# Kernel tuning notes

Measured on AMD Instinct MI355X. Metric: run time of the kernel, lower is better.

The kernel has to match this reference:

```python
import jax, jax.numpy as jnp
import numpy as np

B, S, D = 2, 2048, 768
H = 12
HD = D // H


def setup_inputs() -> dict:
    key = jax.random.key(0)
    k1, k2, k3 = jax.random.split(key, 3)
    hidden_states = jax.random.normal(k1, (B, S, D), dtype=jnp.float32)
    Wqkv = jax.random.normal(k2, (D, 3 * D), dtype=jnp.float32) * (1.0 / np.sqrt(D))
    bqkv = jnp.zeros((3 * D,), dtype=jnp.float32)
    Wout = jax.random.normal(k3, (D, D), dtype=jnp.float32) * (1.0 / np.sqrt(D))
    bout = jnp.zeros((D,), dtype=jnp.float32)
    return {"hidden_states": hidden_states, "Wqkv": Wqkv, "bqkv": bqkv,
            "Wout": Wout, "bout": bout}


def reference(hidden_states, Wqkv, bqkv, Wout, bout):
    b, s, d = hidden_states.shape
    h, hd = H, HD
    scale = hd ** -0.5
    qkv = hidden_states @ Wqkv + bqkv                      # [b, s, 3d]
    q, k, v = jnp.split(qkv, 3, axis=-1)
    # [b, h, s, hd]
    q = q.reshape(b, s, h, hd).transpose(0, 2, 1, 3)
    k = k.reshape(b, s, h, hd).transpose(0, 2, 1, 3)
    v = v.reshape(b, s, h, hd).transpose(0, 2, 1, 3)
    scores = jnp.einsum('bhqd,bhkd->bhqk', q, k) * scale   # [b, h, s, s]
    causal = jnp.tril(jnp.ones((s, s), dtype=bool))
    scores = jnp.where(causal, scores, -jnp.inf)
    attn = jax.nn.softmax(scores, axis=-1)
    out = jnp.einsum('bhqk,bhkd->bhqd', attn, v)           # [b, h, s, hd]
    out = out.transpose(0, 2, 1, 3).reshape(b, s, d)
    return out @ Wout + bout
```

## Files before the change

kernel.cpp:

```cpp
#include <hip/hip_runtime.h>
#include <hip/hip_bf16.h>

typedef __attribute__((ext_vector_type(8))) short bf16x8;
typedef __attribute__((ext_vector_type(4))) float f32x4;
typedef __attribute__((ext_vector_type(4))) unsigned int u32x4;

#define NB 2
#define NS 2048
#define ND 768
#define NH 12
#define NHD 64
#define N3D 2304
#define NM (NB * NS)

__device__ __forceinline__ unsigned short f2bf(float x) {
    union { float f; unsigned u; } v; v.f = x;
    unsigned r = v.u + 0x7FFFu + ((v.u >> 16) & 1u);
    return (unsigned short)(r >> 16);
}

__device__ __forceinline__ unsigned cvt_pk_bf16(float lo, float hi) {
    unsigned r;
    asm volatile("v_cvt_pk_bf16_f32 %0, %1, %2" : "=v"(r) : "v"(lo), "v"(hi));
    return r;
}

__device__ __forceinline__ void transp_tile(const float* __restrict__ in,
                                            unsigned short* __restrict__ out,
                                            int K, int N, int nt, int kt,
                                            float (*T)[33]) {
    const int n0 = nt * 32, k0 = kt * 32;
    const int r = threadIdx.x >> 3, c4 = (threadIdx.x & 7) * 4;
    float4 v = *reinterpret_cast<const float4*>(&in[(size_t)(k0 + r) * N + n0 + c4]);
    T[r][c4 + 0] = v.x; T[r][c4 + 1] = v.y; T[r][c4 + 2] = v.z; T[r][c4 + 3] = v.w;
    __syncthreads();
    ushort4 o;
    o.x = f2bf(T[c4 + 0][r]); o.y = f2bf(T[c4 + 1][r]);
    o.z = f2bf(T[c4 + 2][r]); o.w = f2bf(T[c4 + 3][r]);
    *reinterpret_cast<ushort4*>(&out[(size_t)(n0 + r) * K + k0 + c4]) = o;
}

__global__ __launch_bounds__(256)
void prep(const float* __restrict__ hs, unsigned short* __restrict__ hsb,
          const float* __restrict__ Wqkv, unsigned short* __restrict__ W1t,
          const float* __restrict__ Wout, unsigned short* __restrict__ W2t) {
    __shared__ float T[32][33];
    const int bid = blockIdx.x;
    if (bid < 3072) {
        const int i = (bid * 256 + threadIdx.x) * 4;
        float4 v = *reinterpret_cast<const float4*>(hs + i);
        ushort4 o;
        o.x = f2bf(v.x); o.y = f2bf(v.y); o.z = f2bf(v.z); o.w = f2bf(v.w);
        *reinterpret_cast<ushort4*>(hsb + i) = o;
    } else if (bid < 3072 + 1728) {
        const int idx = bid - 3072;
        transp_tile(Wqkv, W1t, ND, N3D, idx % 72, idx / 72, T);
    } else {
        const int idx = bid - 4800;
        transp_tile(Wout, W2t, ND, ND, idx % 24, idx / 24, T);
    }
}

__global__ __launch_bounds__(256)
void vtransp(const unsigned short* __restrict__ V, unsigned short* __restrict__ Vt) {
    __shared__ __align__(16) unsigned short T[64][72];
    const int bh = blockIdx.y;
    const int s0 = blockIdx.x * 64;
    const int t = threadIdx.x;
    const unsigned short* src = V + ((size_t)bh * NS + s0) * NHD;
    const int r = t >> 2, cc = (t & 3) * 16;
    *(bf16x8*)&T[r][cc]     = *(const bf16x8*)&src[r * NHD + cc];
    *(bf16x8*)&T[r][cc + 8] = *(const bf16x8*)&src[r * NHD + cc + 8];
    __syncthreads();
    unsigned short* dst = Vt + ((size_t)bh * NHD) * NS + s0;
    const int chunk = t & 7;
#pragma unroll
    for (int h = 0; h < 2; ++h) {
        const int d = (t >> 3) + h * 32;
        bf16x8 v;
#pragma unroll
        for (int e = 0; e < 8; ++e) v[e] = (short)T[chunk * 8 + e][d];
        *(bf16x8*)&dst[(size_t)d * NS + chunk * 8] = v;
    }
}

template<int BM, int BN, int EPI>
__global__ __launch_bounds__(256)
void gemm_k768(const unsigned short* __restrict__ A,
               const unsigned short* __restrict__ Bt,
               const float* __restrict__ bias,
               unsigned short* __restrict__ Qo, unsigned short* __restrict__ Ko,
               unsigned short* __restrict__ Vo, float* __restrict__ Co) {
    __shared__ unsigned short As[BM * 64];
    __shared__ unsigned short Bs[BN * 64];
    const int t = threadIdx.x;
    const int wv = t >> 6, lane = t & 63;
    const int lr = lane & 15, lg = lane >> 4;
    const int wr = wv >> 1, wc = wv & 1;
    const int m0 = blockIdx.y * BM;
    const int n0 = blockIdx.x * BN;
    constexpr int FM = BM / 32;
    constexpr int FN = BN / 32;

    f32x4 acc[FM][FN];
#pragma unroll
    for (int i = 0; i < FM; ++i)
#pragma unroll
        for (int j = 0; j < FN; ++j) acc[i][j] = (f32x4){0.f, 0.f, 0.f, 0.f};

    const int sr = t >> 3;
    const int sb = t & 7;

    for (int ki = 0; ki < ND / 64; ++ki) {
        const int k0 = ki * 64;
        __syncthreads();
#pragma unroll
        for (int jj = 0; jj < BM / 32; ++jj) {
            const int row = jj * 32 + sr;
            __builtin_amdgcn_global_load_lds(
                (const void*)(A + (size_t)(m0 + row) * ND + k0 + ((sb ^ (row & 7)) * 8)),
                (void*)(As + jj * 2048 + wv * 512), 16, 0, 0);
        }
#pragma unroll
        for (int jj = 0; jj < BN / 32; ++jj) {
            const int row = jj * 32 + sr;
            __builtin_amdgcn_global_load_lds(
                (const void*)(Bt + (size_t)(n0 + row) * ND + k0 + ((sb ^ (row & 7)) * 8)),
                (void*)(Bs + jj * 2048 + wv * 512), 16, 0, 0);
        }
        __syncthreads();
#pragma unroll
        for (int kc = 0; kc < 2; ++kc) {
            bf16x8 af[FM], bfr[FN];
#pragma unroll
            for (int mi = 0; mi < FM; ++mi) {
                const int row = wr * (BM / 2) + mi * 16 + lr;
                af[mi] = *(const bf16x8*)&As[row * 64 + (((kc * 4 + lg) ^ (row & 7)) * 8)];
            }
#pragma unroll
            for (int nj = 0; nj < FN; ++nj) {
                const int row = wc * (BN / 2) + nj * 16 + lr;
                bfr[nj] = *(const bf16x8*)&Bs[row * 64 + (((kc * 4 + lg) ^ (row & 7)) * 8)];
            }
#pragma unroll
            for (int mi = 0; mi < FM; ++mi)
#pragma unroll
                for (int nj = 0; nj < FN; ++nj)
                    acc[mi][nj] = __builtin_amdgcn_mfma_f32_16x16x32_bf16(
                        af[mi], bfr[nj], acc[mi][nj], 0, 0, 0);
        }
    }

    if (EPI == 0) {
        const int sec = n0 / ND;
#pragma unroll
        for (int mi = 0; mi < FM; ++mi) {
#pragma unroll
            for (int nj = 0; nj < FN; ++nj) {
                const int n = n0 + wc * (BN / 2) + nj * 16 + lr;
                const int rem = n - sec * ND;
                const int hh = rem >> 6, dd = rem & 63;
                const float b = bias[n];
#pragma unroll
                for (int r = 0; r < 4; ++r) {
                    const int m = m0 + wr * (BM / 2) + mi * 16 + lg * 4 + r;
                    const int bb = m >> 11, ss = m & (NS - 1);
                    const int bhh = bb * NH + hh;
                    const float v = acc[mi][nj][r] + b;
                    if (sec == 0)
                        Qo[((size_t)bhh * NS + ss) * NHD + dd] = f2bf(v * 0.18033688011112042f);
                    else if (sec == 1)
                        Ko[((size_t)bhh * NS + ss) * NHD + dd] = f2bf(v);
                    else
                        Vo[((size_t)bhh * NS + ss) * NHD + dd] = f2bf(v);
                }
            }
        }
    } else {
#pragma unroll
        for (int mi = 0; mi < FM; ++mi)
#pragma unroll
            for (int nj = 0; nj < FN; ++nj) {
                const int n = n0 + wc * (BN / 2) + nj * 16 + lr;
                const float b = bias[n];
#pragma unroll
                for (int r = 0; r < 4; ++r) {
                    const int m = m0 + wr * (BM / 2) + mi * 16 + lg * 4 + r;
                    Co[(size_t)m * ND + n] = acc[mi][nj][r] + b;
                }
            }
    }
}

__global__ __launch_bounds__(256)
void attn_mfma(const unsigned short* __restrict__ Qg,
               const unsigned short* __restrict__ Kg,
               const unsigned short* __restrict__ Vtg,
               unsigned short* __restrict__ AO) {
    __shared__ unsigned short Ks[2][64 * 64];
    __shared__ unsigned short Vs[2][64 * 64];
    const int n = blockIdx.x;
    const int x = n & 7, ii = n >> 3;
    const int bh = ((ii >> 5) << 3) + x;
    const int qt = (31 - (ii & 31) + 11 * (ii >> 5)) & 31;
    const int t = threadIdx.x;
    const int w = t >> 6, lane = t & 63;
    const int lr = lane & 15, lg = lane >> 4;
    const int lgp = lg & 1;
    const int qrow = qt * 64 + w * 16 + lr;
    const size_t bhoff = (size_t)bh * (NS * NHD);

    const unsigned short* Qp = Qg + bhoff + (size_t)qrow * NHD;
    const bf16x8 qB0 = *(const bf16x8*)(Qp + lg * 8);
    const bf16x8 qB1 = *(const bf16x8*)(Qp + 32 + lg * 8);

    float m_run = -1e30f, l_part = 0.f;
    f32x4 of[4];
#pragma unroll
    for (int f = 0; f < 4; ++f) of[f] = (f32x4){0.f, 0.f, 0.f, 0.f};

    const unsigned short* Kb = Kg + bhoff;
    const unsigned short* Vb = Vtg + bhoff;
    const int srow = lane >> 3, sblk = lane & 7;
    const int ntiles = qt + 1;
    const int bswz = ((lg & 1) << 1) | (lg >> 1);

#define STAGE(buf, kv0)                                                           \
    {                                                                             \
        _Pragma("unroll")                                                         \
        for (int h = 0; h < 2; ++h) {                                             \
            const int rr = w * 16 + h * 8 + srow;                                 \
            __builtin_amdgcn_global_load_lds(                                     \
                (const void*)(Kb + (size_t)((kv0) + rr) * NHD + ((sblk ^ (rr & 7)) * 8)),  \
                (void*)(Ks[buf] + (w * 16 + h * 8) * 64), 16, 0, 0);              \
            __builtin_amdgcn_global_load_lds(                                     \
                (const void*)(Vb + (size_t)rr * NS + (kv0) + ((sblk ^ (rr & 7)) * 8)),     \
                (void*)(Vs[buf] + (w * 16 + h * 8) * 64), 16, 0, 0);              \
        }                                                                         \
    }

    STAGE(0, 0);
    for (int kt = 0; kt < ntiles; ++kt) {
        __syncthreads();
        if (kt + 1 < ntiles) STAGE((kt + 1) & 1, (kt + 1) * 64);
        const unsigned short* Kc = Ks[kt & 1];
        const unsigned short* Vc = Vs[kt & 1];
        const int kv0 = kt * 64;

        f32x4 sf[4];
#pragma unroll
        for (int f = 0; f < 4; ++f) sf[f] = (f32x4){0.f, 0.f, 0.f, 0.f};
        __builtin_amdgcn_s_setprio(1);
#pragma unroll
        for (int f = 0; f < 4; ++f) {
            const int krow = f * 16 + lr;
            const bf16x8 a0 = *(const bf16x8*)&Kc[krow * 64 + ((lg ^ (krow & 7)) * 8)];
            const bf16x8 a1 = *(const bf16x8*)&Kc[krow * 64 + (((4 + lg) ^ (krow & 7)) * 8)];
            sf[f] = __builtin_amdgcn_mfma_f32_16x16x32_bf16(a0, qB0, sf[f], 0, 0, 0);
            sf[f] = __builtin_amdgcn_mfma_f32_16x16x32_bf16(a1, qB1, sf[f], 0, 0, 0);
        }
        __builtin_amdgcn_s_setprio(0);

        if (kt == ntiles - 1) {
            const int thr = qrow - kv0;
#pragma unroll
            for (int f = 0; f < 4; ++f)
#pragma unroll
                for (int r = 0; r < 4; ++r)
                    if (f * 16 + lg * 4 + r > thr) sf[f][r] = -1e30f;
        }

        float tm = -1e30f;
#pragma unroll
        for (int f = 0; f < 4; ++f)
            tm = fmaxf(tm, fmaxf(fmaxf(sf[f][0], sf[f][1]), fmaxf(sf[f][2], sf[f][3])));
        tm = fmaxf(tm, __shfl_xor(tm, 16));
        tm = fmaxf(tm, __shfl_xor(tm, 32));
        if (!__all(tm <= m_run)) {
            const float nm = fmaxf(m_run, tm);
            const float corr = exp2f(m_run - nm);
            m_run = nm;
            l_part *= corr;
#pragma unroll
            for (int f = 0; f < 4; ++f)
#pragma unroll
                for (int r = 0; r < 4; ++r) of[f][r] *= corr;
        }
#pragma unroll
        for (int f = 0; f < 4; ++f)
#pragma unroll
            for (int r = 0; r < 4; ++r) {
                sf[f][r] = exp2f(sf[f][r] - m_run);
                l_part += sf[f][r];
            }

        bf16x8 pb[2];
#pragma unroll
        for (int c = 0; c < 2; ++c) {
            const unsigned A0 = cvt_pk_bf16(sf[2 * c][0], sf[2 * c][1]);
            const unsigned A1 = cvt_pk_bf16(sf[2 * c][2], sf[2 * c][3]);
            const unsigned B0 = cvt_pk_bf16(sf[2 * c + 1][0], sf[2 * c + 1][1]);
            const unsigned B1 = cvt_pk_bf16(sf[2 * c + 1][2], sf[2 * c + 1][3]);
            const unsigned s0 = lgp ? A0 : B0;
            const unsigned s1 = lgp ? A1 : B1;
            const unsigned r0 = (unsigned)__shfl_xor((int)s0, 16);
            const unsigned r1 = (unsigned)__shfl_xor((int)s1, 16);
            const unsigned o0 = lgp ? B0 : A0;
            const unsigned o1 = lgp ? B1 : A1;
            u32x4 wvv;
            wvv[0] = lgp ? r0 : o0;
            wvv[1] = lgp ? r1 : o1;
            wvv[2] = lgp ? o0 : r0;
            wvv[3] = lgp ? o1 : r1;
            pb[c] = __builtin_bit_cast(bf16x8, wvv);
        }

        __builtin_amdgcn_s_setprio(1);
#pragma unroll
        for (int fA = 0; fA < 4; ++fA) {
            const int drow = fA * 16 + lr;
#pragma unroll
            for (int c = 0; c < 2; ++c) {
                const int blk = 4 * c + bswz;
                const bf16x8 va = *(const bf16x8*)&Vc[drow * 64 + ((blk ^ (drow & 7)) * 8)];
                of[fA] = __builtin_amdgcn_mfma_f32_16x16x32_bf16(va, pb[c], of[fA], 0, 0, 0);
            }
        }
        __builtin_amdgcn_s_setprio(0);
    }
#undef STAGE

    l_part += __shfl_xor(l_part, 16);
    l_part += __shfl_xor(l_part, 32);
    const float inv = 1.f / l_part;
    const int bb = bh / NH, hh = bh - bb * NH;
    unsigned short* op = AO + ((size_t)(bb * NS + qrow)) * ND + hh * NHD;
#pragma unroll
    for (int fA = 0; fA < 4; ++fA) {
        ushort4 o4;
        o4.x = f2bf(of[fA][0] * inv);
        o4.y = f2bf(of[fA][1] * inv);
        o4.z = f2bf(of[fA][2] * inv);
        o4.w = f2bf(of[fA][3] * inv);
        *reinterpret_cast<ushort4*>(op + fA * 16 + lg * 4) = o4;
    }
}

extern "C" void kernel_launch(void* const* d_in, const int* in_sizes, int n_in,
                              void* d_out, int out_size, void* d_ws, size_t ws_size,
                              hipStream_t stream) {
    const float* hs   = (const float*)d_in[0];
    const float* Wqkv = (const float*)d_in[1];
    const float* bqkv = (const float*)d_in[2];
    const float* Wout = (const float*)d_in[3];
    const float* bout = (const float*)d_in[4];
    float* out = (float*)d_out;

    char* wp = (char*)d_ws;
    unsigned short* hsb = (unsigned short*)wp; wp += (size_t)NM * ND * 2;
    unsigned short* W1t = (unsigned short*)wp; wp += (size_t)N3D * ND * 2;
    unsigned short* W2t = (unsigned short*)wp; wp += (size_t)ND * ND * 2;
    const size_t per = (size_t)NB * NH * NS * NHD;
    unsigned short* Qb  = (unsigned short*)wp; wp += per * 2;
    unsigned short* Kb  = (unsigned short*)wp; wp += per * 2;
    unsigned short* Vtb = (unsigned short*)wp; wp += per * 2;
    unsigned short* AOb = (unsigned short*)wp; wp += per * 2;

    prep<<<3072 + 1728 + 576, 256, 0, stream>>>(hs, hsb, Wqkv, W1t, Wout, W2t);

    gemm_k768<128, 128, 0><<<dim3(N3D / 128, NM / 128), 256, 0, stream>>>(
        hsb, W1t, bqkv, Qb, Kb, AOb, nullptr);

    vtransp<<<dim3(NS / 64, NB * NH), 256, 0, stream>>>(AOb, Vtb);

    attn_mfma<<<dim3(NS / 64 * NB * NH), 256, 0, stream>>>(Qb, Kb, Vtb, AOb);

    gemm_k768<64, 64, 1><<<dim3(ND / 64, NM / 64), 256, 0, stream>>>(
        AOb, W2t, bout, nullptr, nullptr, nullptr, out);
}
```

Baseline: 184.5 us.

## Rewrite attention as single-wave blocks with register-resident K/V and 32-row query tiles

```diff
diff --git a/kernel.cpp b/kernel.cpp
--- a/kernel.cpp
+++ b/kernel.cpp
@@ -192,157 +192,177 @@
     }
 }
 
-__global__ __launch_bounds__(256)
+__global__ __launch_bounds__(64)
 void attn_mfma(const unsigned short* __restrict__ Qg,
                const unsigned short* __restrict__ Kg,
                const unsigned short* __restrict__ Vtg,
                unsigned short* __restrict__ AO) {
-    __shared__ unsigned short Ks[2][64 * 64];
-    __shared__ unsigned short Vs[2][64 * 64];
     const int n = blockIdx.x;
     const int x = n & 7, ii = n >> 3;
-    const int bh = ((ii >> 5) << 3) + x;
-    const int qt = (31 - (ii & 31) + 11 * (ii >> 5)) & 31;
-    const int t = threadIdx.x;
-    const int w = t >> 6, lane = t & 63;
+    const int bh = ((ii >> 6) << 3) + x;
+    const int j = ii & 63;
+    const int qb = (j < 32) ? (2 * j) : (63 - 2 * (j - 32));
+    const int lane = threadIdx.x;
     const int lr = lane & 15, lg = lane >> 4;
     const int lgp = lg & 1;
-    const int qrow = qt * 64 + w * 16 + lr;
+    const int q0 = qb * 32;
     const size_t bhoff = (size_t)bh * (NS * NHD);
-
-    const unsigned short* Qp = Qg + bhoff + (size_t)qrow * NHD;
-    const bf16x8 qB0 = *(const bf16x8*)(Qp + lg * 8);
-    const bf16x8 qB1 = *(const bf16x8*)(Qp + 32 + lg * 8);
-
-    float m_run = -1e30f, l_part = 0.f;
-    f32x4 of[4];
-#pragma unroll
-    for (int f = 0; f < 4; ++f) of[f] = (f32x4){0.f, 0.f, 0.f, 0.f};
-
     const unsigned short* Kb = Kg + bhoff;
     const unsigned short* Vb = Vtg + bhoff;
-    const int srow = lane >> 3, sblk = lane & 7;
-    const int ntiles = qt + 1;
     const int bswz = ((lg & 1) << 1) | (lg >> 1);
 
-#define STAGE(buf, kv0)                                                           \
-    {                                                                             \
-        _Pragma("unroll")                                                         \
-        for (int h = 0; h < 2; ++h) {                                             \
-            const int rr = w * 16 + h * 8 + srow;                                 \
-            __builtin_amdgcn_global_load_lds(                                     \
-                (const void*)(Kb + (size_t)((kv0) + rr) * NHD + ((sblk ^ (rr & 7)) * 8)),  \
-                (void*)(Ks[buf] + (w * 16 + h * 8) * 64), 16, 0, 0);              \
-            __builtin_amdgcn_global_load_lds(                                     \
-                (const void*)(Vb + (size_t)rr * NS + (kv0) + ((sblk ^ (rr & 7)) * 8)),     \
-                (void*)(Vs[buf] + (w * 16 + h * 8) * 64), 16, 0, 0);              \
-        }                                                                         \
-    }
-
-    STAGE(0, 0);
-    for (int kt = 0; kt < ntiles; ++kt) {
-        __syncthreads();
-        if (kt + 1 < ntiles) STAGE((kt + 1) & 1, (kt + 1) * 64);
-        const unsigned short* Kc = Ks[kt & 1];
-        const unsigned short* Vc = Vs[kt & 1];
-        const int kv0 = kt * 64;
-
-        f32x4 sf[4];
-#pragma unroll
-        for (int f = 0; f < 4; ++f) sf[f] = (f32x4){0.f, 0.f, 0.f, 0.f};
-        __builtin_amdgcn_s_setprio(1);
-#pragma unroll
-        for (int f = 0; f < 4; ++f) {
-            const int krow = f * 16 + lr;
-            const bf16x8 a0 = *(const bf16x8*)&Kc[krow * 64 + ((lg ^ (krow & 7)) * 8)];
-            const bf16x8 a1 = *(const bf16x8*)&Kc[krow * 64 + (((4 + lg) ^ (krow & 7)) * 8)];
-            sf[f] = __builtin_amdgcn_mfma_f32_16x16x32_bf16(a0, qB0, sf[f], 0, 0, 0);
-            sf[f] = __builtin_amdgcn_mfma_f32_16x16x32_bf16(a1, qB1, sf[f], 0, 0, 0);
+    bf16x8 qB[2][2];
+#pragma unroll
+    for (int qf = 0; qf < 2; ++qf)
+#pragma unroll
+        for (int c = 0; c < 2; ++c)
+            qB[qf][c] = *(const bf16x8*)(Qg + bhoff +
+                (size_t)(q0 + qf * 16 + lr) * NHD + c * 32 + lg * 8);
+
+    float m_run[2] = {-1e30f, -1e30f}, l_part[2] = {0.f, 0.f};
+    f32x4 of[4][2];
+#pragma unroll
+    for (int f = 0; f < 4; ++f)
+#pragma unroll
+        for (int qf = 0; qf < 2; ++qf) of[f][qf] = (f32x4){0.f, 0.f, 0.f, 0.f};
+
+    const int ntiles = qb / 2 + 1;
+
+#define LOADK(KB, kv0)                                                          \
+    {                                                                           \
+        _Pragma("unroll")                                                       \
+        for (int f = 0; f < 4; ++f)                                             \
+            _Pragma("unroll")                                                   \
+            for (int c = 0; c < 2; ++c)                                         \
+                KB[f][c] = *(const bf16x8*)(Kb +                                \
+                    (size_t)((kv0) + f * 16 + lr) * NHD + c * 32 + lg * 8);     \
+    }
+
+#define TILE_BODY(KCUR, KNEXT, kt)                                             \
+    {                                                                          \
+        const int kv0 = (kt) * 64;                                             \
+        f32x4 sf[4][2];                                                        \
+        _Pragma("unroll")                                                      \
+        for (int f = 0; f < 4; ++f)                                            \
+            _Pragma("unroll")                                                  \
+            for (int qf = 0; qf < 2; ++qf) sf[f][qf] = (f32x4){0.f,0.f,0.f,0.f}; \
+        __builtin_amdgcn_s_setprio(1);                                         \
+        _Pragma("unroll")                                                      \
+        for (int f = 0; f < 4; ++f)                                            \
+            _Pragma("unroll")                                                  \
+            for (int c = 0; c < 2; ++c)                                        \
+                _Pragma("unroll")                                              \
+                for (int qf = 0; qf < 2; ++qf)                                 \
+                    sf[f][qf] = __builtin_amdgcn_mfma_f32_16x16x32_bf16(       \
+                        KCUR[f][c], qB[qf][c], sf[f][qf], 0, 0, 0);            \
+        __builtin_amdgcn_s_setprio(0);                                         \
+        if ((kt) + 1 < ntiles) LOADK(KNEXT, kv0 + 64);                         \
+        bf16x8 vv[4][2];                                                       \
+        _Pragma("unroll")                                                      \
+        for (int fA = 0; fA < 4; ++fA)                                         \
+            _Pragma("unroll")                                                  \
+            for (int c = 0; c < 2; ++c)                                        \
+                vv[fA][c] = *(const bf16x8*)(Vb +                              \
+                    (size_t)(fA * 16 + lr) * NS + kv0 + (4 * c + bswz) * 8);   \
+        if ((kt) == ntiles - 1) {                                              \
+            _Pragma("unroll")                                                  \
+            for (int qf = 0; qf < 2; ++qf) {                                   \
+                const int thr = q0 + qf * 16 + lr - kv0;                       \
+                _Pragma("unroll")                                              \
+                for (int f = 0; f < 4; ++f)                                    \
+                    _Pragma("unroll")                                          \
+                    for (int r = 0; r < 4; ++r)                                \
+                        if (f * 16 + lg * 4 + r > thr) sf[f][qf][r] = -1e30f;  \
+            }                                                                  \
+        }                                                                      \
+        bf16x8 pb[2][2];                                                       \
+        _Pragma("unroll")                                                      \
+        for (int qf = 0; qf < 2; ++qf) {                                       \
+            float tm = -1e30f;                                                 \
+            _Pragma("unroll")                                                  \
+            for (int f = 0; f < 4; ++f)                                        \
+                tm = fmaxf(tm, fmaxf(fmaxf(sf[f][qf][0], sf[f][qf][1]),        \
+                                     fmaxf(sf[f][qf][2], sf[f][qf][3])));      \
+            tm = fmaxf(tm, __shfl_xor(tm, 16));                                \
+            tm = fmaxf(tm, __shfl_xor(tm, 32));                                \
+            if (!__all(tm <= m_run[qf])) {                                     \
+                const float nm = fmaxf(m_run[qf], tm);                         \
+                const float corr = exp2f(m_run[qf] - nm);                      \
+                m_run[qf] = nm;                                                \
+                l_part[qf] *= corr;                                            \
+                _Pragma("unroll")                                              \
+                for (int f = 0; f < 4; ++f)                                    \
+                    _Pragma("unroll")                                          \
+                    for (int r = 0; r < 4; ++r) of[f][qf][r] *= corr;          \
+            }                                                                  \
+            _Pragma("unroll")                                                  \
+            for (int f = 0; f < 4; ++f)                                        \
+                _Pragma("unroll")                                              \
+                for (int r = 0; r < 4; ++r) {                                  \
+                    sf[f][qf][r] = exp2f(sf[f][qf][r] - m_run[qf]);            \
+                    l_part[qf] += sf[f][qf][r];                                \
+                }                                                              \
+            _Pragma("unroll")                                                  \
+            for (int c = 0; c < 2; ++c) {                                      \
+                const unsigned A0 = cvt_pk_bf16(sf[2*c][qf][0], sf[2*c][qf][1]);   \
+                const unsigned A1 = cvt_pk_bf16(sf[2*c][qf][2], sf[2*c][qf][3]);   \
+                const unsigned B0 = cvt_pk_bf16(sf[2*c+1][qf][0], sf[2*c+1][qf][1]); \
+                const unsigned B1 = cvt_pk_bf16(sf[2*c+1][qf][2], sf[2*c+1][qf][3]); \
+                const unsigned s0 = lgp ? A0 : B0;                             \
+                const unsigned s1 = lgp ? A1 : B1;                             \
+                const unsigned r0 = (unsigned)__shfl_xor((int)s0, 16);         \
+                const unsigned r1 = (unsigned)__shfl_xor((int)s1, 16);         \
+                const unsigned o0 = lgp ? B0 : A0;                             \
+                const unsigned o1 = lgp ? B1 : A1;                             \
+                u32x4 wvv;                                                     \
+                wvv[0] = lgp ? r0 : o0;                                        \
+                wvv[1] = lgp ? r1 : o1;                                        \
+                wvv[2] = lgp ? o0 : r0;                                        \
+                wvv[3] = lgp ? o1 : r1;                                        \
+                pb[qf][c] = __builtin_bit_cast(bf16x8, wvv);                   \
+            }                                                                  \
+        }                                                                      \
+        __builtin_amdgcn_s_setprio(1);                                         \
+        _Pragma("unroll")                                                      \
+        for (int fA = 0; fA < 4; ++fA)                                         \
+            _Pragma("unroll")                                                  \
+            for (int c = 0; c < 2; ++c)                                        \
+                _Pragma("unroll")                                              \
+                for (int qf = 0; qf < 2; ++qf)                                 \
+                    of[fA][qf] = __builtin_amdgcn_mfma_f32_16x16x32_bf16(      \
+                        vv[fA][c], pb[qf][c], of[fA][qf], 0, 0, 0);            \
+        __builtin_amdgcn_s_setprio(0);                                         \
+    }
+
+    bf16x8 kA[4][2], kB_[4][2];
+    LOADK(kA, 0);
+    int kt = 0;
+    while (true) {
+        TILE_BODY(kA, kB_, kt);
+        if (++kt == ntiles) break;
+        TILE_BODY(kB_, kA, kt);
+        if (++kt == ntiles) break;
+    }
+#undef TILE_BODY
+#undef LOADK
+
+    const int bb = bh / NH, hh = bh - bb * NH;
+#pragma unroll
+    for (int qf = 0; qf < 2; ++qf) {
+        float l = l_part[qf];
+        l += __shfl_xor(l, 16);
+        l += __shfl_xor(l, 32);
+        const float inv = 1.f / l;
+        unsigned short* op = AO + ((size_t)(bb * NS + q0 + qf * 16 + lr)) * ND + hh * NHD;
+#pragma unroll
+        for (int fA = 0; fA < 4; ++fA) {
+            ushort4 o4;
+            o4.x = f2bf(of[fA][qf][0] * inv);
+            o4.y = f2bf(of[fA][qf][1] * inv);
+            o4.z = f2bf(of[fA][qf][2] * inv);
+            o4.w = f2bf(of[fA][qf][3] * inv);
+            *reinterpret_cast<ushort4*>(op + fA * 16 + lg * 4) = o4;
         }
-        __builtin_amdgcn_s_setprio(0);
-
-        if (kt == ntiles - 1) {
-            const int thr = qrow - kv0;
-#pragma unroll
-            for (int f = 0; f < 4; ++f)
-#pragma unroll
-                for (int r = 0; r < 4; ++r)
-                    if (f * 16 + lg * 4 + r > thr) sf[f][r] = -1e30f;
-        }
-
-        float tm = -1e30f;
-#pragma unroll
-        for (int f = 0; f < 4; ++f)
-            tm = fmaxf(tm, fmaxf(fmaxf(sf[f][0], sf[f][1]), fmaxf(sf[f][2], sf[f][3])));
-        tm = fmaxf(tm, __shfl_xor(tm, 16));
-        tm = fmaxf(tm, __shfl_xor(tm, 32));
-        if (!__all(tm <= m_run)) {
-            const float nm = fmaxf(m_run, tm);
-            const float corr = exp2f(m_run - nm);
-            m_run = nm;
-            l_part *= corr;
-#pragma unroll
-            for (int f = 0; f < 4; ++f)
-#pragma unroll
-                for (int r = 0; r < 4; ++r) of[f][r] *= corr;
-        }
-#pragma unroll
-        for (int f = 0; f < 4; ++f)
-#pragma unroll
-            for (int r = 0; r < 4; ++r) {
-                sf[f][r] = exp2f(sf[f][r] - m_run);
-                l_part += sf[f][r];
-            }
-
-        bf16x8 pb[2];
-#pragma unroll
-        for (int c = 0; c < 2; ++c) {
-            const unsigned A0 = cvt_pk_bf16(sf[2 * c][0], sf[2 * c][1]);
-            const unsigned A1 = cvt_pk_bf16(sf[2 * c][2], sf[2 * c][3]);
-            const unsigned B0 = cvt_pk_bf16(sf[2 * c + 1][0], sf[2 * c + 1][1]);
-            const unsigned B1 = cvt_pk_bf16(sf[2 * c + 1][2], sf[2 * c + 1][3]);
-            const unsigned s0 = lgp ? A0 : B0;
-            const unsigned s1 = lgp ? A1 : B1;
-            const unsigned r0 = (unsigned)__shfl_xor((int)s0, 16);
-            const unsigned r1 = (unsigned)__shfl_xor((int)s1, 16);
-            const unsigned o0 = lgp ? B0 : A0;
-            const unsigned o1 = lgp ? B1 : A1;
-            u32x4 wvv;
-            wvv[0] = lgp ? r0 : o0;
-            wvv[1] = lgp ? r1 : o1;
-            wvv[2] = lgp ? o0 : r0;
-            wvv[3] = lgp ? o1 : r1;
-            pb[c] = __builtin_bit_cast(bf16x8, wvv);
-        }
-
-        __builtin_amdgcn_s_setprio(1);
-#pragma unroll
-        for (int fA = 0; fA < 4; ++fA) {
-            const int drow = fA * 16 + lr;
-#pragma unroll
-            for (int c = 0; c < 2; ++c) {
-                const int blk = 4 * c + bswz;
-                const bf16x8 va = *(const bf16x8*)&Vc[drow * 64 + ((blk ^ (drow & 7)) * 8)];
-                of[fA] = __builtin_amdgcn_mfma_f32_16x16x32_bf16(va, pb[c], of[fA], 0, 0, 0);
-            }
-        }
-        __builtin_amdgcn_s_setprio(0);
-    }
-#undef STAGE
-
-    l_part += __shfl_xor(l_part, 16);
-    l_part += __shfl_xor(l_part, 32);
-    const float inv = 1.f / l_part;
-    const int bb = bh / NH, hh = bh - bb * NH;
-    unsigned short* op = AO + ((size_t)(bb * NS + qrow)) * ND + hh * NHD;
-#pragma unroll
-    for (int fA = 0; fA < 4; ++fA) {
-        ushort4 o4;
-        o4.x = f2bf(of[fA][0] * inv);
-        o4.y = f2bf(of[fA][1] * inv);
-        o4.z = f2bf(of[fA][2] * inv);
-        o4.w = f2bf(of[fA][3] * inv);
-        *reinterpret_cast<ushort4*>(op + fA * 16 + lg * 4) = o4;
     }
 }
 
@@ -373,7 +393,7 @@
 
     vtransp<<<dim3(NS / 64, NB * NH), 256, 0, stream>>>(AOb, Vtb);
 
-    attn_mfma<<<dim3(NS / 64 * NB * NH), 256, 0, stream>>>(Qb, Kb, Vtb, AOb);
+    attn_mfma<<<NS / 32 * NB * NH, 64, 0, stream>>>(Qb, Kb, Vtb, AOb);
 
     gemm_k768<64, 64, 1><<<dim3(ND / 64, NM / 64), 256, 0, stream>>>(
         AOb, W2t, bout, nullptr, nullptr, nullptr, out);
```

After: 203.4 us. +10.2%, slower.

## Fuse V transpose into QKV GEMM epilogue via LDS staging

Applied to the files above, without the earlier changes.

```diff
diff --git a/kernel.cpp b/kernel.cpp
--- a/kernel.cpp
+++ b/kernel.cpp
@@ -61,38 +61,16 @@
     }
 }
 
-__global__ __launch_bounds__(256)
-void vtransp(const unsigned short* __restrict__ V, unsigned short* __restrict__ Vt) {
-    __shared__ __align__(16) unsigned short T[64][72];
-    const int bh = blockIdx.y;
-    const int s0 = blockIdx.x * 64;
-    const int t = threadIdx.x;
-    const unsigned short* src = V + ((size_t)bh * NS + s0) * NHD;
-    const int r = t >> 2, cc = (t & 3) * 16;
-    *(bf16x8*)&T[r][cc]     = *(const bf16x8*)&src[r * NHD + cc];
-    *(bf16x8*)&T[r][cc + 8] = *(const bf16x8*)&src[r * NHD + cc + 8];
-    __syncthreads();
-    unsigned short* dst = Vt + ((size_t)bh * NHD) * NS + s0;
-    const int chunk = t & 7;
-#pragma unroll
-    for (int h = 0; h < 2; ++h) {
-        const int d = (t >> 3) + h * 32;
-        bf16x8 v;
-#pragma unroll
-        for (int e = 0; e < 8; ++e) v[e] = (short)T[chunk * 8 + e][d];
-        *(bf16x8*)&dst[(size_t)d * NS + chunk * 8] = v;
-    }
-}
-
 template<int BM, int BN, int EPI>
 __global__ __launch_bounds__(256)
 void gemm_k768(const unsigned short* __restrict__ A,
                const unsigned short* __restrict__ Bt,
                const float* __restrict__ bias,
                unsigned short* __restrict__ Qo, unsigned short* __restrict__ Ko,
-               unsigned short* __restrict__ Vo, float* __restrict__ Co) {
-    __shared__ unsigned short As[BM * 64];
-    __shared__ unsigned short Bs[BN * 64];
+               unsigned short* __restrict__ Vto, float* __restrict__ Co) {
+    __shared__ unsigned short SMEM[(BM + BN) * 64];
+    unsigned short* As = SMEM;
+    unsigned short* Bs = SMEM + BM * 64;
     const int t = threadIdx.x;
     const int wv = t >> 6, lane = t & 63;
     const int lr = lane & 15, lg = lane >> 4;
@@ -153,27 +131,60 @@
 
     if (EPI == 0) {
         const int sec = n0 / ND;
-#pragma unroll
-        for (int mi = 0; mi < FM; ++mi) {
-#pragma unroll
-            for (int nj = 0; nj < FN; ++nj) {
-                const int n = n0 + wc * (BN / 2) + nj * 16 + lr;
-                const int rem = n - sec * ND;
+        if (sec < 2) {
+#pragma unroll
+            for (int mi = 0; mi < FM; ++mi) {
+#pragma unroll
+                for (int nj = 0; nj < FN; ++nj) {
+                    const int n = n0 + wc * (BN / 2) + nj * 16 + lr;
+                    const int rem = n - sec * ND;
+                    const int hh = rem >> 6, dd = rem & 63;
+                    const float b = bias[n];
+#pragma unroll
+                    for (int r = 0; r < 4; ++r) {
+                        const int m = m0 + wr * (BM / 2) + mi * 16 + lg * 4 + r;
+                        const int bb = m >> 11, ss = m & (NS - 1);
+                        const int bhh = bb * NH + hh;
+                        const float v = acc[mi][nj][r] + b;
+                        if (sec == 0)
+                            Qo[((size_t)bhh * NS + ss) * NHD + dd] = f2bf(v * 0.18033688011112042f);
+                        else
+                            Ko[((size_t)bhh * NS + ss) * NHD + dd] = f2bf(v);
+                    }
+                }
+            }
+        } else {
+            __syncthreads();
+            char* Tb = reinterpret_cast<char*>(SMEM);
+#pragma unroll
+            for (int mi = 0; mi < FM; ++mi) {
+#pragma unroll
+                for (int nj = 0; nj < FN; ++nj) {
+                    const int n_l = wc * (BN / 2) + nj * 16 + lr;
+                    const int m_l = wr * (BM / 2) + mi * 16 + lg * 4;
+                    const float b = bias[n0 + n_l];
+                    ushort4 pk;
+                    pk.x = f2bf(acc[mi][nj][0] + b);
+                    pk.y = f2bf(acc[mi][nj][1] + b);
+                    pk.z = f2bf(acc[mi][nj][2] + b);
+                    pk.w = f2bf(acc[mi][nj][3] + b);
+                    const int off = n_l * 256 + (((m_l * 2) ^ ((n_l & 15) << 4)));
+                    *reinterpret_cast<ushort4*>(Tb + off) = pk;
+                }
+            }
+            __syncthreads();
+            const int bb = m0 >> 11;
+            const int ssb = m0 & (NS - 1);
+#pragma unroll
+            for (int h = 0; h < (BN * 16) / 256; ++h) {
+                const int p = t + 256 * h;
+                const int n_l = p >> 4, j = p & 15;
+                const int off = n_l * 256 + (((j ^ (n_l & 15)) << 4));
+                bf16x8 v = *reinterpret_cast<const bf16x8*>(Tb + off);
+                const int rem = n0 + n_l - 2 * ND;
                 const int hh = rem >> 6, dd = rem & 63;
-                const float b = bias[n];
-#pragma unroll
-                for (int r = 0; r < 4; ++r) {
-                    const int m = m0 + wr * (BM / 2) + mi * 16 + lg * 4 + r;
-                    const int bb = m >> 11, ss = m & (NS - 1);
-                    const int bhh = bb * NH + hh;
-                    const float v = acc[mi][nj][r] + b;
-                    if (sec == 0)
-                        Qo[((size_t)bhh * NS + ss) * NHD + dd] = f2bf(v * 0.18033688011112042f);
-                    else if (sec == 1)
-                        Ko[((size_t)bhh * NS + ss) * NHD + dd] = f2bf(v);
-                    else
-                        Vo[((size_t)bhh * NS + ss) * NHD + dd] = f2bf(v);
-                }
+                const int bhh = bb * NH + hh;
+                *reinterpret_cast<bf16x8*>(Vto + ((size_t)(bhh * NHD + dd)) * NS + ssb + 8 * j) = v;
             }
         }
     } else {
@@ -368,10 +379,8 @@
 
     prep<<<3072 + 1728 + 576, 256, 0, stream>>>(hs, hsb, Wqkv, W1t, Wout, W2t);
 
-    gemm_k768<128, 128, 0><<<dim3(N3D / 128, NM / 128), 256, 0, stream>>>(
-        hsb, W1t, bqkv, Qb, Kb, AOb, nullptr);
-
-    vtransp<<<dim3(NS / 64, NB * NH), 256, 0, stream>>>(AOb, Vtb);
+    gemm_k768<128, 96, 0><<<dim3(N3D / 96, NM / 128), 256, 0, stream>>>(
+        hsb, W1t, bqkv, Qb, Kb, Vtb, nullptr);
 
     attn_mfma<<<dim3(NS / 64 * NB * NH), 256, 0, stream>>>(Qb, Kb, Vtb, AOb);
 
```

After: 165.7 us. 1.11x faster.
